# Kernel optimization log

Measured on AMD Instinct MI355X. Metric: run time of the kernel, lower is better.

## Reference

```python
import jax, jax.numpy as jnp
import numpy as np

D = 512  # d_model
B, H, W = 32, 32, 32


def _conv1x1(x, w, b):
    # x: [B,C,H,W], w: [O,C], b: [O] -> [B,O,H,W]
    return jnp.einsum('oc,bchw->bohw', w, x) + b[None, :, None, None]


def setup_inputs() -> dict:
    key = jax.random.key(0)
    ks = jax.random.split(key, 16)
    std = 0.01  # init.normal_(m.weight, 0, 0.01)
    inp = {
        'out0': jax.random.normal(ks[0], (B, D, H, W), jnp.float32),
        'out1': jax.random.normal(ks[1], (B, D, H, W), jnp.float32),
        'out2': jax.random.normal(ks[2], (B, D, H, W), jnp.float32),
        'gamma': jax.random.uniform(ks[3], (1,), jnp.float32),
        'gamma_1': jax.random.uniform(ks[4], (1,), jnp.float32),
        'gamma_2': jax.random.uniform(ks[5], (1,), jnp.float32),
        'W_in1': std * jax.random.normal(ks[6], (D, D), jnp.float32),
        'b_in1': jnp.zeros((D,), jnp.float32),
        'W_in2': std * jax.random.normal(ks[7], (D, D), jnp.float32),
        'b_in2': jnp.zeros((D,), jnp.float32),
        'W_in3': std * jax.random.normal(ks[8], (D, D), jnp.float32),
        'b_in3': jnp.zeros((D,), jnp.float32),
        'W_trans': std * jax.random.normal(ks[9], (3 * D, 3 * D), jnp.float32),
        'b_trans': jnp.zeros((3 * D,), jnp.float32),
        'W_out1': std * jax.random.normal(ks[10], (D, D), jnp.float32),
        'b_out1': jnp.zeros((D,), jnp.float32),
        'W_out2': std * jax.random.normal(ks[11], (D, D), jnp.float32),
        'b_out2': jnp.zeros((D,), jnp.float32),
        'W_out3': std * jax.random.normal(ks[12], (D, D), jnp.float32),
        'b_out3': jnp.zeros((D,), jnp.float32),
    }
    return inp


def reference(out0, out1, out2, gamma, gamma_1, gamma_2,
              W_in1, b_in1, W_in2, b_in2, W_in3, b_in3,
              W_trans, b_trans, W_out1, b_out1, W_out2, b_out2,
              W_out3, b_out3):
    out_sim = gamma[0] * out0
    out_sim_1 = gamma_1[0] * out1
    out_sim_2 = gamma_2[0] * out2
    H_1 = _conv1x1(out_sim, W_in1, b_in1)
    H_2 = _conv1x1(out_sim_1, W_in2, b_in2)
    H_3 = _conv1x1(out_sim_2, W_in3, b_in3)
    H_cat = jnp.concatenate((H_1, H_2, H_3), axis=1)  # [B,3D,H,W]
    H_tra = _conv1x1(H_cat, W_trans, b_trans)
    s0, s1, s2 = H_tra[:, :D], H_tra[:, D:2 * D], H_tra[:, 2 * D:]
    H_4 = jax.nn.sigmoid(_conv1x1(s0, W_out1, b_out1))
    H_5 = jax.nn.sigmoid(_conv1x1(s1, W_out2, b_out2))
    H_6 = jax.nn.sigmoid(_conv1x1(s2, W_out3, b_out3))
    H_st = jnp.stack((H_4, H_5, H_6), axis=0)  # [3,B,D,H,W]
    H_all = jax.nn.softmax(H_st, axis=0)
    fused = H_all[0] * out_sim + H_all[1] * out_sim_1 + H_all[2] * out_sim_2
    return fused
```

## Files before the change

### kernel.cpp

```cpp
#include <hip/hip_runtime.h>
#include <hip/hip_bf16.h>

#define NPIX 32768
#define DCH 512
#define HWSZ 1024
#define WSQ (DCH * DCH)
#define WTR (3 * DCH * 3 * DCH)

typedef __bf16 bf16x8_t __attribute__((ext_vector_type(8)));
typedef float f32x4_t __attribute__((ext_vector_type(4)));
typedef float f32x16_t __attribute__((ext_vector_type(16)));
typedef int i32x4_t __attribute__((ext_vector_type(4)));
typedef int i32x8_t __attribute__((ext_vector_type(8)));
typedef unsigned short u16x8_t __attribute__((ext_vector_type(8)));
typedef unsigned short u16x4_t __attribute__((ext_vector_type(4)));

static __device__ __forceinline__ unsigned short f2bf(float f) {
    return __builtin_bit_cast(unsigned short, __float2bfloat16(f));
}
static __device__ __forceinline__ float bf2f(unsigned short u) {
    unsigned v = (unsigned)u << 16;
    return __builtin_bit_cast(float, v);
}

__global__ __launch_bounds__(256)
void cvt_all(const float* __restrict__ w0, const float* __restrict__ w1,
             const float* __restrict__ w2, const float* __restrict__ w3,
             const float* __restrict__ w4, const float* __restrict__ w5,
             const float* __restrict__ w6, __hip_bfloat16* __restrict__ d,
             const float* __restrict__ b0, const float* __restrict__ b1,
             const float* __restrict__ b2, const float* __restrict__ b3,
             const float* __restrict__ b4, const float* __restrict__ b5,
             float* __restrict__ biasd)
{
    if (blockIdx.x == gridDim.x - 1) {
        for (int idx = threadIdx.x; idx < 3072; idx += 256) {
            const int r = idx >> 9, off = idx & 511;
            const float* s = (r == 0) ? b0 : (r == 1) ? b1 : (r == 2) ? b2
                           : (r == 3) ? b3 : (r == 4) ? b4 : b5;
            biasd[idx] = s[off];
        }
        return;
    }
    const int i = (blockIdx.x * 256 + threadIdx.x) * 4;
    if (i < 3 * WSQ) {
        int r = i >> 18;
        const float* src = (r == 0) ? w0 : ((r == 1) ? w1 : w2);
        int off = i - r * WSQ;
        float4 f = *(const float4*)(src + off);
        u16x4_t v;
        v[0] = f2bf(f.x); v[1] = f2bf(f.y); v[2] = f2bf(f.z); v[3] = f2bf(f.w);
        *(u16x4_t*)((unsigned short*)d + i) = v;
    } else if (i < 3 * WSQ + WTR) {
        int off = i - 3 * WSQ;
        float4 f = *(const float4*)(w3 + off);
        int dw = __builtin_amdgcn_cvt_pk_fp8_f32(f.x, f.y, 0, false);
        dw     = __builtin_amdgcn_cvt_pk_fp8_f32(f.z, f.w, dw, true);
        unsigned char* d8 = (unsigned char*)(d + 3 * WSQ);
        *(int*)(d8 + off) = dw;
    } else {
        int j = i - 3 * WSQ - WTR;
        int r = j >> 18;
        const float* src = (r == 0) ? w4 : ((r == 1) ? w5 : w6);
        int off = j - r * WSQ;
        float4 f = *(const float4*)(src + off);
        u16x4_t v;
        v[0] = f2bf(f.x); v[1] = f2bf(f.y); v[2] = f2bf(f.z); v[3] = f2bf(f.w);
        *(u16x4_t*)((unsigned short*)d + i) = v;
    }
}

__global__ __launch_bounds__(256)
void stage_transpose(const float* __restrict__ x0, const float* __restrict__ x1,
                     const float* __restrict__ x2,
                     const float* __restrict__ gp0, const float* __restrict__ gp1,
                     const float* __restrict__ gp2,
                     __hip_bfloat16* __restrict__ XbT)
{
    __shared__ float tile[64][65];
    const int hw0 = blockIdx.x * 64;
    const int c0  = blockIdx.y * 64;
    const int bz  = blockIdx.z;
    const int br  = bz >> 5;
    const int b   = bz & 31;
    const float* x = (br == 0) ? x0 : ((br == 1) ? x1 : x2);
    const float g  = ((br == 0) ? gp0 : ((br == 1) ? gp1 : gp2))[0];
    const int t = threadIdx.x;

    const int hwi = t & 63;
    const int cb  = t >> 6;
    const float* src = x + (size_t)b * (DCH * HWSZ) + (size_t)c0 * HWSZ + hw0;
#pragma unroll
    for (int i = 0; i < 16; ++i) {
        const int ci = cb + i * 4;
        tile[ci][hwi] = g * src[(size_t)ci * HWSZ + hwi];
    }
    __syncthreads();

    const int hwr = t >> 2;
    const int cch = (t & 3) * 16;
    __hip_bfloat16* dst = XbT + (size_t)((size_t)br * NPIX + b * HWSZ + hw0 + hwr) * DCH + c0 + cch;
    u16x8_t v0, v1;
#pragma unroll
    for (int e = 0; e < 8; ++e) v0[e] = f2bf(tile[cch + e][hwr]);
#pragma unroll
    for (int e = 0; e < 8; ++e) v1[e] = f2bf(tile[cch + 8 + e][hwr]);
    *(u16x8_t*)dst = v0;
    *((u16x8_t*)dst + 1) = v1;
}

__global__ __launch_bounds__(512, 2)
void gemm256(const __hip_bfloat16* __restrict__ A, int lda,
             const __hip_bfloat16* __restrict__ B, int ldb,
             const float* __restrict__ bias,
             __hip_bfloat16* __restrict__ C, int ldc, int coff0,
             int K, int NO, int TPB, int brA, int brB, int bstride,
             int cstride, int trans_out, int cmode)
{
    __shared__ __align__(16) unsigned char smem[131072];
    const int tid  = threadIdx.x;
    const int lane = tid & 63;
    const int wave = tid >> 6;
    const int wm   = wave >> 2;
    const int wn   = wave & 3;
    const int l16  = lane & 15;
    const int l4   = lane >> 4;

    const int per  = gridDim.x >> 3;
    const int flat = (blockIdx.x & 7) * per + (blockIdx.x >> 3);
    const int br   = flat / TPB;
    const int rem  = flat - br * TPB;
    const int nt   = rem / NO;
    const int ot   = rem - nt * NO;
    const int n0 = nt * 256;
    const int o0 = ot * 256;
    const int NT = K >> 6;

    A    += (size_t)br * (size_t)brA;
    B    += (size_t)br * (size_t)brB;
    bias += br * bstride;
    const int coff = coff0 + br * cstride;

    const unsigned xorv = (unsigned)((l16 & 7) << 4);
    unsigned baseA[2], baseB[2];
#pragma unroll
    for (int kk = 0; kk < 2; ++kk) {
        const unsigned ko = ((unsigned)(kk * 64 + l4 * 16)) ^ xorv;
        baseA[kk] = (unsigned)((wm * 128 + l16) * 128) + ko;
        baseB[kk] = 32768u + (unsigned)((wn * 64 + l16) * 128) + ko;
    }

    const int rr  = lane >> 3;
    const int kel = 8 * ((lane & 7) ^ rr);

    auto stageA = [&](int t, int half) {
        const unsigned dst = (unsigned)((t & 1) * 65536 + half * 16384 + wave * 2048);
        const __hip_bfloat16* g = A + (size_t)(n0 + half * 128 + wave * 16 + rr) * lda + t * 64 + kel;
#pragma unroll
        for (int s = 0; s < 2; ++s) {
            __builtin_amdgcn_global_load_lds(
                (const __attribute__((address_space(1))) unsigned int*)(g + (size_t)s * 8 * lda),
                (__attribute__((address_space(3))) unsigned int*)(smem + dst + s * 1024),
                16, 0, 0);
        }
    };
    auto stageB = [&](int t, int half) {
        const unsigned dst = (unsigned)((t & 1) * 65536 + 32768 + half * 16384 + wave * 2048);
        const __hip_bfloat16* g = B + (size_t)(o0 + half * 128 + wave * 16 + rr) * ldb + t * 64 + kel;
#pragma unroll
        for (int s = 0; s < 2; ++s) {
            __builtin_amdgcn_global_load_lds(
                (const __attribute__((address_space(1))) unsigned int*)(g + (size_t)s * 8 * ldb),
                (__attribute__((address_space(3))) unsigned int*)(smem + dst + s * 1024),
                16, 0, 0);
        }
    };

#define DSRO(dst, addr, OFF) \
    asm volatile("ds_read_b128 %0, %1 offset:" #OFF : "=v"(dst) : "v"(addr))
#define BC(x) __builtin_bit_cast(bf16x8_t, x)

    stageA(0, 0); stageA(0, 1); stageB(0, 0); stageB(0, 1);
    stageA(1, 0); stageA(1, 1); stageB(1, 0); stageB(1, 1);
    asm volatile("s_waitcnt vmcnt(8)");
    __builtin_amdgcn_s_barrier();

    f32x4_t aR[4][2], a2[4][2], bA[2][2], bB[2][2];
    f32x4_t acc[8][4];
#pragma unroll
    for (int m = 0; m < 8; ++m)
#pragma unroll
        for (int n = 0; n < 4; ++n) acc[m][n] = (f32x4_t){0.f, 0.f, 0.f, 0.f};

    {
        unsigned a0 = baseA[0], a1 = baseA[1], b0 = baseB[0], b1 = baseB[1];
        DSRO(aR[0][0], a0, 0);    DSRO(aR[1][0], a0, 2048);
        DSRO(aR[2][0], a0, 4096); DSRO(aR[3][0], a0, 6144);
        DSRO(aR[0][1], a1, 0);    DSRO(aR[1][1], a1, 2048);
        DSRO(aR[2][1], a1, 4096); DSRO(aR[3][1], a1, 6144);
        DSRO(bA[0][0], b0, 0);    DSRO(bA[1][0], b0, 2048);
        DSRO(bA[0][1], b1, 0);    DSRO(bA[1][1], b1, 2048);
    }

    unsigned cb = 0;
    for (int t = 0; t < NT; ++t) {
        const unsigned cbn = cb ^ 65536u;
        const unsigned a0 = cb + baseA[0], a1 = cb + baseA[1];
        const unsigned b0 = cb + baseB[0], b1 = cb + baseB[1];

        asm volatile("s_waitcnt lgkmcnt(0)");
        __builtin_amdgcn_sched_barrier(0);
        DSRO(bB[0][0], b0, 4096); DSRO(bB[1][0], b0, 6144);
        DSRO(bB[0][1], b1, 4096); DSRO(bB[1][1], b1, 6144);
        __builtin_amdgcn_sched_barrier(0);
        __builtin_amdgcn_s_setprio(1);
#pragma unroll
        for (int m = 0; m < 4; ++m)
#pragma unroll
            for (int n = 0; n < 2; ++n)
#pragma unroll
                for (int kk = 0; kk < 2; ++kk)
                    acc[m][n] = __builtin_amdgcn_mfma_f32_16x16x32_bf16(BC(aR[m][kk]), BC(bA[n][kk]), acc[m][n], 0, 0, 0);
        __builtin_amdgcn_s_setprio(0);
        __builtin_amdgcn_s_barrier();

        asm volatile("s_waitcnt lgkmcnt(0)");
        __builtin_amdgcn_sched_barrier(0);
        DSRO(a2[0][0], a0, 8192);  DSRO(a2[1][0], a0, 10240);
        DSRO(a2[2][0], a0, 12288); DSRO(a2[3][0], a0, 14336);
        DSRO(a2[0][1], a1, 8192);  DSRO(a2[1][1], a1, 10240);
        DSRO(a2[2][1], a1, 12288); DSRO(a2[3][1], a1, 14336);
        __builtin_amdgcn_sched_barrier(0);
        __builtin_amdgcn_s_setprio(1);
#pragma unroll
        for (int m = 0; m < 4; ++m)
#pragma unroll
            for (int n = 0; n < 2; ++n)
#pragma unroll
                for (int kk = 0; kk < 2; ++kk)
                    acc[m][n + 2] = __builtin_amdgcn_mfma_f32_16x16x32_bf16(BC(aR[m][kk]), BC(bB[n][kk]), acc[m][n + 2], 0, 0, 0);
        __builtin_amdgcn_s_setprio(0);
        __builtin_amdgcn_s_barrier();

        asm volatile("s_waitcnt lgkmcnt(0)");
        __builtin_amdgcn_sched_barrier(0);
        if (t + 2 < NT) { stageB(t + 2, 0); stageB(t + 2, 1); }
        __builtin_amdgcn_sched_barrier(0);
        __builtin_amdgcn_s_setprio(1);
#pragma unroll
        for (int m = 0; m < 4; ++m)
#pragma unroll
            for (int n = 0; n < 2; ++n)
#pragma unroll
                for (int kk = 0; kk < 2; ++kk)
                    acc[m + 4][n] = __builtin_amdgcn_mfma_f32_16x16x32_bf16(BC(a2[m][kk]), BC(bA[n][kk]), acc[m + 4][n], 0, 0, 0);
        __builtin_amdgcn_s_setprio(0);
        if (t + 2 < NT)        { asm volatile("s_waitcnt vmcnt(4)"); }
        else if (t + 2 == NT)  { asm volatile("s_waitcnt vmcnt(0)"); }
        __builtin_amdgcn_s_barrier();

        if (t + 1 < NT) {
            const unsigned na0 = cbn + baseA[0], na1 = cbn + baseA[1];
            const unsigned nb0 = cbn + baseB[0], nb1 = cbn + baseB[1];
            DSRO(aR[0][0], na0, 0);    DSRO(aR[1][0], na0, 2048);
            DSRO(aR[2][0], na0, 4096); DSRO(aR[3][0], na0, 6144);
            DSRO(aR[0][1], na1, 0);    DSRO(aR[1][1], na1, 2048);
            DSRO(aR[2][1], na1, 4096); DSRO(aR[3][1], na1, 6144);
            DSRO(bA[0][0], nb0, 0);    DSRO(bA[1][0], nb0, 2048);
            DSRO(bA[0][1], nb1, 0);    DSRO(bA[1][1], nb1, 2048);
        }
        if (t + 2 < NT) { stageA(t + 2, 0); stageA(t + 2, 1); }
        __builtin_amdgcn_sched_barrier(0);
        __builtin_amdgcn_s_setprio(1);
#pragma unroll
        for (int m = 0; m < 4; ++m)
#pragma unroll
            for (int n = 0; n < 2; ++n)
#pragma unroll
                for (int kk = 0; kk < 2; ++kk)
                    acc[m + 4][n + 2] = __builtin_amdgcn_mfma_f32_16x16x32_bf16(BC(a2[m][kk]), BC(bB[n][kk]), acc[m + 4][n + 2], 0, 0, 0);
        __builtin_amdgcn_s_setprio(0);
        cb = cbn;
    }

    if (!trans_out) {
        if (cmode == 1) {
            unsigned char* C8 = (unsigned char*)C;
#pragma unroll
            for (int n = 0; n < 4; ++n) {
                const int oc = o0 + wn * 64 + n * 16 + l16;
                const float bv = bias[oc];
#pragma unroll
                for (int m = 0; m < 8; ++m) {
                    int dw = __builtin_amdgcn_cvt_pk_fp8_f32(acc[m][n][0] + bv, acc[m][n][1] + bv, 0, false);
                    dw     = __builtin_amdgcn_cvt_pk_fp8_f32(acc[m][n][2] + bv, acc[m][n][3] + bv, dw, true);
                    const int nr = n0 + wm * 128 + m * 16 + l4 * 4;
                    const size_t base = (size_t)nr * ldc + coff + oc;
                    const unsigned u = (unsigned)dw;
                    C8[base]           = (unsigned char)u;
                    C8[base + ldc]     = (unsigned char)(u >> 8);
                    C8[base + 2 * ldc] = (unsigned char)(u >> 16);
                    C8[base + 3 * ldc] = (unsigned char)(u >> 24);
                }
            }
        } else {
#pragma unroll
            for (int n = 0; n < 4; ++n) {
                const int oc = o0 + wn * 64 + n * 16 + l16;
                const float bv = bias[oc];
#pragma unroll
                for (int m = 0; m < 8; ++m)
#pragma unroll
                    for (int r = 0; r < 4; ++r) {
                        const int nr = n0 + wm * 128 + m * 16 + l4 * 4 + r;
                        C[(size_t)nr * ldc + coff + oc] = __float2bfloat16(acc[m][n][r] + bv);
                    }
            }
        }
    } else {
        __syncthreads();
#pragma unroll
        for (int n = 0; n < 4; ++n) {
            const int ocl = wn * 64 + n * 16 + l16;
            const float bv = bias[o0 + ocl];
#pragma unroll
            for (int m = 0; m < 8; ++m)
#pragma unroll
                for (int r = 0; r < 4; ++r) {
                    const int nrow = wm * 128 + m * 16 + l4 * 4 + r;
                    const unsigned phys = (unsigned)nrow * 512u
                        + (((unsigned)ocl * 2u) ^ (((unsigned)(nrow & 7)) << 4));
                    *(unsigned short*)(smem + phys) = f2bf(acc[m][n][r] + bv);
                }
        }
        __syncthreads();
        const int ol = tid >> 1;
        const int nh = (tid & 1) * 128;
        __hip_bfloat16* dst = C + (size_t)(coff + o0 + ol) * ldc + n0 + nh;
#pragma unroll
        for (int j8 = 0; j8 < 16; ++j8) {
            u16x8_t v;
#pragma unroll
            for (int e = 0; e < 8; ++e) {
                const int n2 = nh + j8 * 8 + e;
                v[e] = *(const unsigned short*)(smem + (unsigned)n2 * 512u
                        + ((((unsigned)ol * 2u) ^ ((unsigned)e << 4))));
            }
            *(u16x8_t*)((unsigned short*)dst + j8 * 8) = v;
        }
    }
#undef DSRO
#undef BC
}

__global__ __launch_bounds__(256, 3)
void gemm_f8(const unsigned char* __restrict__ A, int lda,
             const unsigned char* __restrict__ B, int ldb,
             const float* __restrict__ bias,
             __hip_bfloat16* __restrict__ C, int ldc,
             int K, int NO)
{
    __shared__ __align__(16) unsigned char smem[32768];
    const int tid  = threadIdx.x;
    const int lane = tid & 63;
    const int wave = tid >> 6;
    const int wm = wave >> 1, wn = wave & 1;
    const int l31 = lane & 31;
    const int h   = lane >> 5;

    const int per  = gridDim.x >> 3;
    const int flat = (blockIdx.x & 7) * per + (blockIdx.x >> 3);
    const int nt = flat / NO, ot = flat % NO;
    const int n0 = nt * 128, o0 = ot * 128;
    const int NT = K >> 6;

    auto stage = [&](int t, unsigned bufb) {
#pragma unroll
        for (int p = 0; p < 2; ++p) {
            const int f   = tid + p * 256;
            const int row = f >> 2, cidx = f & 3;
            const int gch = ((cidx ^ (row & 3) ^ ((row >> 2) & 3)) << 4);
            const unsigned char* ga = A + (size_t)(n0 + row) * lda + t * 64 + gch;
            __builtin_amdgcn_global_load_lds(
                (const __attribute__((address_space(1))) unsigned int*)ga,
                (__attribute__((address_space(3))) unsigned int*)(smem + bufb + f * 16),
                16, 0, 0);
            const unsigned char* gb = B + (size_t)(o0 + row) * ldb + t * 64 + gch;
            __builtin_amdgcn_global_load_lds(
                (const __attribute__((address_space(1))) unsigned int*)gb,
                (__attribute__((address_space(3))) unsigned int*)(smem + bufb + 8192u + f * 16),
                16, 0, 0);
        }
    };

    f32x16_t acc[2][2];
#pragma unroll
    for (int mf = 0; mf < 2; ++mf)
#pragma unroll
        for (int nf = 0; nf < 2; ++nf)
#pragma unroll
            for (int e = 0; e < 16; ++e) acc[mf][nf][e] = 0.f;

    stage(0, 0);
    __syncthreads();

    for (int t = 0; t < NT; ++t) {
        const unsigned bb = (unsigned)((t & 1) << 14);
        if (t + 1 < NT) stage(t + 1, bb ^ 16384u);

        i32x8_t af[2], bf[2];
#pragma unroll
        for (int mf = 0; mf < 2; ++mf) {
            const int r = wm * 64 + mf * 32 + l31;
            const int s = (r & 3) ^ ((r >> 2) & 3);
            const unsigned base = bb + (unsigned)(r << 6);
            i32x4_t lo = *(const i32x4_t*)(smem + base + ((((h << 1) | 0) ^ s) << 4));
            i32x4_t hi = *(const i32x4_t*)(smem + base + ((((h << 1) | 1) ^ s) << 4));
            af[mf][0] = lo[0]; af[mf][1] = lo[1]; af[mf][2] = lo[2]; af[mf][3] = lo[3];
            af[mf][4] = hi[0]; af[mf][5] = hi[1]; af[mf][6] = hi[2]; af[mf][7] = hi[3];
        }
#pragma unroll
        for (int nf = 0; nf < 2; ++nf) {
            const int r = wn * 64 + nf * 32 + l31;
            const int s = (r & 3) ^ ((r >> 2) & 3);
            const unsigned base = bb + 8192u + (unsigned)(r << 6);
            i32x4_t lo = *(const i32x4_t*)(smem + base + ((((h << 1) | 0) ^ s) << 4));
            i32x4_t hi = *(const i32x4_t*)(smem + base + ((((h << 1) | 1) ^ s) << 4));
            bf[nf][0] = lo[0]; bf[nf][1] = lo[1]; bf[nf][2] = lo[2]; bf[nf][3] = lo[3];
            bf[nf][4] = hi[0]; bf[nf][5] = hi[1]; bf[nf][6] = hi[2]; bf[nf][7] = hi[3];
        }
#pragma unroll
        for (int mf = 0; mf < 2; ++mf)
#pragma unroll
            for (int nf = 0; nf < 2; ++nf)
                acc[mf][nf] = __builtin_amdgcn_mfma_scale_f32_32x32x64_f8f6f4(
                    af[mf], bf[nf], acc[mf][nf],
                    0, 0,
                    0, 0x7F7F7F7F,
                    0, 0x7F7F7F7F);
        __syncthreads();
    }

#pragma unroll
    for (int nf = 0; nf < 2; ++nf) {
        const int col = o0 + wn * 64 + nf * 32 + l31;
        const float bv = bias[col];
#pragma unroll
        for (int mf = 0; mf < 2; ++mf)
#pragma unroll
            for (int rg = 0; rg < 16; ++rg) {
                const int row = n0 + wm * 64 + mf * 32 + (rg & 3) + ((rg >> 2) << 3) + (h << 2);
                C[(size_t)row * ldc + col] = __float2bfloat16(acc[mf][nf][rg] + bv);
            }
    }
}

__global__ __launch_bounds__(256)
void final_v2(const __hip_bfloat16* __restrict__ G,
              const __hip_bfloat16* __restrict__ Xb,
              float* __restrict__ out)
{
    __shared__ float tile[64][68];
    const int n0  = blockIdx.x * 64;
    const int b   = n0 >> 10;
    const int hw0 = n0 & (HWSZ - 1);
    const int t   = threadIdx.x;
    const int nl  = t >> 2;
    const int cg  = (t & 3) * 16;
    const int n   = n0 + nl;
    const unsigned short* gr = (const unsigned short*)G + (size_t)n * 1536;
    const unsigned short* xr = (const unsigned short*)Xb + (size_t)n * 512;
    const int seg = t & 3;
    float* outb = out + (size_t)b * (DCH * HWSZ) + hw0;

    for (int c0 = 0; c0 < DCH; c0 += 64) {
        u16x8_t gl[3][2], xl[3][2];
#pragma unroll
        for (int i = 0; i < 3; ++i) {
            gl[i][0] = *(const u16x8_t*)(gr + i * 512 + c0 + cg);
            gl[i][1] = *(const u16x8_t*)(gr + i * 512 + c0 + cg + 8);
            xl[i][0] = *(const u16x8_t*)(xr + (size_t)i * NPIX * 512 + c0 + cg);
            xl[i][1] = *(const u16x8_t*)(xr + (size_t)i * NPIX * 512 + c0 + cg + 8);
        }
#pragma unroll
        for (int e = 0; e < 16; ++e) {
            const int hh = e >> 3, w = e & 7;
            const float s0 = bf2f(gl[0][hh][w]);
            const float s1 = bf2f(gl[1][hh][w]);
            const float s2 = bf2f(gl[2][hh][w]);
            const float g0 = 1.0f / (1.0f + __expf(-s0));
            const float g1 = 1.0f / (1.0f + __expf(-s1));
            const float g2 = 1.0f / (1.0f + __expf(-s2));
            const float e0 = __expf(g0), e1 = __expf(g1), e2 = __expf(g2);
            const float inv = 1.0f / (e0 + e1 + e2);
            tile[cg + e][nl] = inv * (e0 * bf2f(xl[0][hh][w])
                                    + e1 * bf2f(xl[1][hh][w])
                                    + e2 * bf2f(xl[2][hh][w]));
        }
        __syncthreads();
#pragma unroll
        for (int j4 = 0; j4 < 4; ++j4) {
            float4 v = *(const float4*)&tile[nl][seg * 16 + j4 * 4];
            *(float4*)(outb + (size_t)(c0 + nl) * HWSZ + seg * 16 + j4 * 4) = v;
        }
        __syncthreads();
    }
}

__global__ __launch_bounds__(256)
void final_fuse(const __hip_bfloat16* __restrict__ G,
                const float* __restrict__ x0, const float* __restrict__ x1,
                const float* __restrict__ x2,
                const float* __restrict__ gp0, const float* __restrict__ gp1,
                const float* __restrict__ gp2,
                float* __restrict__ out)
{
    const int n  = blockIdx.x * 256 + threadIdx.x;
    const int b  = n >> 10;
    const int hw = n & (HWSZ - 1);
    const int c0 = blockIdx.y * 64;
    const float ga0 = gp0[0], ga1 = gp1[0], ga2 = gp2[0];
    for (int cc = 0; cc < 64; ++cc) {
        const int c = c0 + cc;
        const float s0 = __bfloat162float(G[(size_t)c * NPIX + n]);
        const float s1 = __bfloat162float(G[(size_t)(c + DCH) * NPIX + n]);
        const float s2 = __bfloat162float(G[(size_t)(c + 2 * DCH) * NPIX + n]);
        const float g0v = 1.0f / (1.0f + __expf(-s0));
        const float g1v = 1.0f / (1.0f + __expf(-s1));
        const float g2v = 1.0f / (1.0f + __expf(-s2));
        const float e0 = __expf(g0v), e1 = __expf(g1v), e2 = __expf(g2v);
        const float inv = 1.0f / (e0 + e1 + e2);
        const size_t xo = (size_t)b * (DCH * HWSZ) + (size_t)c * HWSZ + hw;
        out[xo] = inv * (e0 * ga0 * x0[xo] + e1 * ga1 * x1[xo] + e2 * ga2 * x2[xo]);
    }
}

extern "C" void kernel_launch(void* const* d_in, const int* in_sizes, int n_in,
                              void* d_out, int out_size, void* d_ws, size_t ws_size,
                              hipStream_t stream)
{
    const float* out0   = (const float*)d_in[0];
    const float* out1   = (const float*)d_in[1];
    const float* out2   = (const float*)d_in[2];
    const float* gamma0 = (const float*)d_in[3];
    const float* gamma1 = (const float*)d_in[4];
    const float* gamma2 = (const float*)d_in[5];
    const float* W_in1  = (const float*)d_in[6];
    const float* W_in2  = (const float*)d_in[8];
    const float* W_in3  = (const float*)d_in[10];
    const float* b_in1  = (const float*)d_in[7];
    const float* b_in2  = (const float*)d_in[9];
    const float* b_in3  = (const float*)d_in[11];
    const float* W_tr   = (const float*)d_in[12];
    const float* b_tr   = (const float*)d_in[13];
    const float* W_o1   = (const float*)d_in[14];
    const float* b_o1   = (const float*)d_in[15];
    const float* W_o2   = (const float*)d_in[16];
    const float* b_o2   = (const float*)d_in[17];
    const float* W_o3   = (const float*)d_in[18];
    const float* b_o3   = (const float*)d_in[19];
    float* outp = (float*)d_out;

    unsigned char* ws = (unsigned char*)d_ws;
    const size_t SZ_ACT   = (size_t)3 * NPIX * DCH * 2;
    const size_t WB_BYTES = (size_t)(6 * WSQ + WTR) * 2;
    const size_t NEED3    = 3 * SZ_ACT + WB_BYTES + 4096 * 4;
    const bool   big      = (ws_size >= NEED3);

    __hip_bfloat16* buf0 = (__hip_bfloat16*)ws;
    __hip_bfloat16* buf1 = (__hip_bfloat16*)(ws + SZ_ACT);
    __hip_bfloat16* buf2 = big ? (__hip_bfloat16*)(ws + 2 * SZ_ACT) : buf0;
    unsigned char*  wtop = ws + (big ? 3 : 2) * SZ_ACT;
    __hip_bfloat16* Wb     = (__hip_bfloat16*)wtop;
    __hip_bfloat16* Wb_tr  = Wb + 3 * WSQ;
    unsigned char*  Wtr8   = (unsigned char*)Wb_tr;
    __hip_bfloat16* Wb_o   = Wb_tr + WTR;
    float*          biasWS = (float*)(wtop + WB_BYTES);

    const int CVT_TOTAL = 6 * WSQ + WTR;
    cvt_all<<<CVT_TOTAL / 1024 + 1, 256, 0, stream>>>(
        W_in1, W_in2, W_in3, W_tr, W_o1, W_o2, W_o3, Wb,
        b_in1, b_in2, b_in3, b_o1, b_o2, b_o3, biasWS);

    stage_transpose<<<dim3(16, 8, 96), 256, 0, stream>>>(out0, out1, out2,
                                                         gamma0, gamma1, gamma2, buf0);

    gemm256<<<dim3(768), 512, 0, stream>>>(
        buf0, DCH, Wb, DCH, biasWS,
        buf1, 3 * DCH, 0, DCH, 2, 256, NPIX * DCH, WSQ, DCH, DCH, 0, 1);

    gemm_f8<<<dim3((NPIX / 128) * 12), 256, 0, stream>>>(
        (const unsigned char*)buf1, 3 * DCH, Wtr8, 3 * DCH, b_tr,
        buf2, 3 * DCH, 3 * DCH, 12);

    if (big) {
        gemm256<<<dim3(768), 512, 0, stream>>>(
            buf2, 3 * DCH, Wb_o, DCH, biasWS + 3 * DCH,
            buf1, 3 * DCH, 0, DCH, 2, 256, DCH, WSQ, DCH, DCH, 0, 0);
        final_v2<<<dim3(NPIX / 64), 256, 0, stream>>>(buf1, buf0, outp);
    } else {
        gemm256<<<dim3(768), 512, 0, stream>>>(
            buf0, 3 * DCH, Wb_o, DCH, biasWS + 3 * DCH,
            buf1, NPIX, 0, DCH, 2, 256, DCH, WSQ, DCH, DCH, 1, 0);
        final_fuse<<<dim3(NPIX / 256, DCH / 64), 256, 0, stream>>>(
            buf1, out0, out1, out2, gamma0, gamma1, gamma2, outp);
    }
}
```

Before: 380.9 us.

## Run all three GEMM stages in FP8 with a triple-buffered fp8 GEMM

After: 325.1 us. -14.6%, faster.

```diff
diff --git a/kernel.cpp b/kernel.cpp
--- a/kernel.cpp
+++ b/kernel.cpp
@@ -27,13 +27,16 @@
 void cvt_all(const float* __restrict__ w0, const float* __restrict__ w1,
              const float* __restrict__ w2, const float* __restrict__ w3,
              const float* __restrict__ w4, const float* __restrict__ w5,
-             const float* __restrict__ w6, __hip_bfloat16* __restrict__ d,
+             const float* __restrict__ w6,
+             __hip_bfloat16* __restrict__ d, unsigned char* __restrict__ d8,
              const float* __restrict__ b0, const float* __restrict__ b1,
              const float* __restrict__ b2, const float* __restrict__ b3,
              const float* __restrict__ b4, const float* __restrict__ b5,
              float* __restrict__ biasd)
 {
-    if (blockIdx.x == gridDim.x - 1) {
+    const int NB = (6 * WSQ + WTR) >> 10;
+    const int bid = blockIdx.x;
+    if (bid == 2 * NB) {
         for (int idx = threadIdx.x; idx < 3072; idx += 256) {
             const int r = idx >> 9, off = idx & 511;
             const float* s = (r == 0) ? b0 : (r == 1) ? b1 : (r == 2) ? b2
@@ -42,28 +45,28 @@
         }
         return;
     }
-    const int i = (blockIdx.x * 256 + threadIdx.x) * 4;
+    const bool do8 = (bid >= NB);
+    const int i = ((do8 ? bid - NB : bid) * 256 + threadIdx.x) * 4;
+    const float* src;
+    int off;
     if (i < 3 * WSQ) {
         int r = i >> 18;
-        const float* src = (r == 0) ? w0 : ((r == 1) ? w1 : w2);
-        int off = i - r * WSQ;
-        float4 f = *(const float4*)(src + off);
-        u16x4_t v;
-        v[0] = f2bf(f.x); v[1] = f2bf(f.y); v[2] = f2bf(f.z); v[3] = f2bf(f.w);
-        *(u16x4_t*)((unsigned short*)d + i) = v;
+        src = (r == 0) ? w0 : ((r == 1) ? w1 : w2);
+        off = i - r * WSQ;
     } else if (i < 3 * WSQ + WTR) {
-        int off = i - 3 * WSQ;
-        float4 f = *(const float4*)(w3 + off);
-        int dw = __builtin_amdgcn_cvt_pk_fp8_f32(f.x, f.y, 0, false);
-        dw     = __builtin_amdgcn_cvt_pk_fp8_f32(f.z, f.w, dw, true);
-        unsigned char* d8 = (unsigned char*)(d + 3 * WSQ);
-        *(int*)(d8 + off) = dw;
+        src = w3; off = i - 3 * WSQ;
     } else {
         int j = i - 3 * WSQ - WTR;
         int r = j >> 18;
-        const float* src = (r == 0) ? w4 : ((r == 1) ? w5 : w6);
-        int off = j - r * WSQ;
-        float4 f = *(const float4*)(src + off);
+        src = (r == 0) ? w4 : ((r == 1) ? w5 : w6);
+        off = j - r * WSQ;
+    }
+    float4 f = *(const float4*)(src + off);
+    if (do8) {
+        int dw = __builtin_amdgcn_cvt_pk_fp8_f32(f.x, f.y, 0, false);
+        dw     = __builtin_amdgcn_cvt_pk_fp8_f32(f.z, f.w, dw, true);
+        *(int*)(d8 + i) = dw;
+    } else {
         u16x4_t v;
         v[0] = f2bf(f.x); v[1] = f2bf(f.y); v[2] = f2bf(f.z); v[3] = f2bf(f.w);
         *(u16x4_t*)((unsigned short*)d + i) = v;
@@ -75,7 +78,8 @@
                      const float* __restrict__ x2,
                      const float* __restrict__ gp0, const float* __restrict__ gp1,
                      const float* __restrict__ gp2,
-                     __hip_bfloat16* __restrict__ XbT)
+                     __hip_bfloat16* __restrict__ XbT,
+                     unsigned char* __restrict__ Xb8, int emit8)
 {
     __shared__ float tile[64][65];
     const int hw0 = blockIdx.x * 64;
@@ -99,7 +103,8 @@
 
     const int hwr = t >> 2;
     const int cch = (t & 3) * 16;
-    __hip_bfloat16* dst = XbT + (size_t)((size_t)br * NPIX + b * HWSZ + hw0 + hwr) * DCH + c0 + cch;
+    const size_t nrow = (size_t)br * NPIX + b * HWSZ + hw0 + hwr;
+    __hip_bfloat16* dst = XbT + nrow * DCH + c0 + cch;
     u16x8_t v0, v1;
 #pragma unroll
     for (int e = 0; e < 8; ++e) v0[e] = f2bf(tile[cch + e][hwr]);
@@ -107,260 +112,30 @@
     for (int e = 0; e < 8; ++e) v1[e] = f2bf(tile[cch + 8 + e][hwr]);
     *(u16x8_t*)dst = v0;
     *((u16x8_t*)dst + 1) = v1;
-}
-
-__global__ __launch_bounds__(512, 2)
-void gemm256(const __hip_bfloat16* __restrict__ A, int lda,
-             const __hip_bfloat16* __restrict__ B, int ldb,
-             const float* __restrict__ bias,
-             __hip_bfloat16* __restrict__ C, int ldc, int coff0,
-             int K, int NO, int TPB, int brA, int brB, int bstride,
-             int cstride, int trans_out, int cmode)
-{
-    __shared__ __align__(16) unsigned char smem[131072];
-    const int tid  = threadIdx.x;
-    const int lane = tid & 63;
-    const int wave = tid >> 6;
-    const int wm   = wave >> 2;
-    const int wn   = wave & 3;
-    const int l16  = lane & 15;
-    const int l4   = lane >> 4;
-
-    const int per  = gridDim.x >> 3;
-    const int flat = (blockIdx.x & 7) * per + (blockIdx.x >> 3);
-    const int br   = flat / TPB;
-    const int rem  = flat - br * TPB;
-    const int nt   = rem / NO;
-    const int ot   = rem - nt * NO;
-    const int n0 = nt * 256;
-    const int o0 = ot * 256;
-    const int NT = K >> 6;
-
-    A    += (size_t)br * (size_t)brA;
-    B    += (size_t)br * (size_t)brB;
-    bias += br * bstride;
-    const int coff = coff0 + br * cstride;
-
-    const unsigned xorv = (unsigned)((l16 & 7) << 4);
-    unsigned baseA[2], baseB[2];
-#pragma unroll
-    for (int kk = 0; kk < 2; ++kk) {
-        const unsigned ko = ((unsigned)(kk * 64 + l4 * 16)) ^ xorv;
-        baseA[kk] = (unsigned)((wm * 128 + l16) * 128) + ko;
-        baseB[kk] = 32768u + (unsigned)((wn * 64 + l16) * 128) + ko;
-    }
-
-    const int rr  = lane >> 3;
-    const int kel = 8 * ((lane & 7) ^ rr);
-
-    auto stageA = [&](int t, int half) {
-        const unsigned dst = (unsigned)((t & 1) * 65536 + half * 16384 + wave * 2048);
-        const __hip_bfloat16* g = A + (size_t)(n0 + half * 128 + wave * 16 + rr) * lda + t * 64 + kel;
-#pragma unroll
-        for (int s = 0; s < 2; ++s) {
-            __builtin_amdgcn_global_load_lds(
-                (const __attribute__((address_space(1))) unsigned int*)(g + (size_t)s * 8 * lda),
-                (__attribute__((address_space(3))) unsigned int*)(smem + dst + s * 1024),
-                16, 0, 0);
-        }
-    };
-    auto stageB = [&](int t, int half) {
-        const unsigned dst = (unsigned)((t & 1) * 65536 + 32768 + half * 16384 + wave * 2048);
-        const __hip_bfloat16* g = B + (size_t)(o0 + half * 128 + wave * 16 + rr) * ldb + t * 64 + kel;
-#pragma unroll
-        for (int s = 0; s < 2; ++s) {
-            __builtin_amdgcn_global_load_lds(
-                (const __attribute__((address_space(1))) unsigned int*)(g + (size_t)s * 8 * ldb),
-                (__attribute__((address_space(3))) unsigned int*)(smem + dst + s * 1024),
-                16, 0, 0);
-        }
-    };
-
-#define DSRO(dst, addr, OFF) \
-    asm volatile("ds_read_b128 %0, %1 offset:" #OFF : "=v"(dst) : "v"(addr))
-#define BC(x) __builtin_bit_cast(bf16x8_t, x)
-
-    stageA(0, 0); stageA(0, 1); stageB(0, 0); stageB(0, 1);
-    stageA(1, 0); stageA(1, 1); stageB(1, 0); stageB(1, 1);
-    asm volatile("s_waitcnt vmcnt(8)");
-    __builtin_amdgcn_s_barrier();
-
-    f32x4_t aR[4][2], a2[4][2], bA[2][2], bB[2][2];
-    f32x4_t acc[8][4];
-#pragma unroll
-    for (int m = 0; m < 8; ++m)
-#pragma unroll
-        for (int n = 0; n < 4; ++n) acc[m][n] = (f32x4_t){0.f, 0.f, 0.f, 0.f};
-
-    {
-        unsigned a0 = baseA[0], a1 = baseA[1], b0 = baseB[0], b1 = baseB[1];
-        DSRO(aR[0][0], a0, 0);    DSRO(aR[1][0], a0, 2048);
-        DSRO(aR[2][0], a0, 4096); DSRO(aR[3][0], a0, 6144);
-        DSRO(aR[0][1], a1, 0);    DSRO(aR[1][1], a1, 2048);
-        DSRO(aR[2][1], a1, 4096); DSRO(aR[3][1], a1, 6144);
-        DSRO(bA[0][0], b0, 0);    DSRO(bA[1][0], b0, 2048);
-        DSRO(bA[0][1], b1, 0);    DSRO(bA[1][1], b1, 2048);
-    }
-
-    unsigned cb = 0;
-    for (int t = 0; t < NT; ++t) {
-        const unsigned cbn = cb ^ 65536u;
-        const unsigned a0 = cb + baseA[0], a1 = cb + baseA[1];
-        const unsigned b0 = cb + baseB[0], b1 = cb + baseB[1];
-
-        asm volatile("s_waitcnt lgkmcnt(0)");
-        __builtin_amdgcn_sched_barrier(0);
-        DSRO(bB[0][0], b0, 4096); DSRO(bB[1][0], b0, 6144);
-        DSRO(bB[0][1], b1, 4096); DSRO(bB[1][1], b1, 6144);
-        __builtin_amdgcn_sched_barrier(0);
-        __builtin_amdgcn_s_setprio(1);
-#pragma unroll
-        for (int m = 0; m < 4; ++m)
-#pragma unroll
-            for (int n = 0; n < 2; ++n)
-#pragma unroll
-                for (int kk = 0; kk < 2; ++kk)
-                    acc[m][n] = __builtin_amdgcn_mfma_f32_16x16x32_bf16(BC(aR[m][kk]), BC(bA[n][kk]), acc[m][n], 0, 0, 0);
-        __builtin_amdgcn_s_setprio(0);
-        __builtin_amdgcn_s_barrier();
-
-        asm volatile("s_waitcnt lgkmcnt(0)");
-        __builtin_amdgcn_sched_barrier(0);
-        DSRO(a2[0][0], a0, 8192);  DSRO(a2[1][0], a0, 10240);
-        DSRO(a2[2][0], a0, 12288); DSRO(a2[3][0], a0, 14336);
-        DSRO(a2[0][1], a1, 8192);  DSRO(a2[1][1], a1, 10240);
-        DSRO(a2[2][1], a1, 12288); DSRO(a2[3][1], a1, 14336);
-        __builtin_amdgcn_sched_barrier(0);
-        __builtin_amdgcn_s_setprio(1);
-#pragma unroll
-        for (int m = 0; m < 4; ++m)
-#pragma unroll
-            for (int n = 0; n < 2; ++n)
-#pragma unroll
-                for (int kk = 0; kk < 2; ++kk)
-                    acc[m][n + 2] = __builtin_amdgcn_mfma_f32_16x16x32_bf16(BC(aR[m][kk]), BC(bB[n][kk]), acc[m][n + 2], 0, 0, 0);
-        __builtin_amdgcn_s_setprio(0);
-        __builtin_amdgcn_s_barrier();
-
-        asm volatile("s_waitcnt lgkmcnt(0)");
-        __builtin_amdgcn_sched_barrier(0);
-        if (t + 2 < NT) { stageB(t + 2, 0); stageB(t + 2, 1); }
-        __builtin_amdgcn_sched_barrier(0);
-        __builtin_amdgcn_s_setprio(1);
-#pragma unroll
-        for (int m = 0; m < 4; ++m)
-#pragma unroll
-            for (int n = 0; n < 2; ++n)
-#pragma unroll
-                for (int kk = 0; kk < 2; ++kk)
-                    acc[m + 4][n] = __builtin_amdgcn_mfma_f32_16x16x32_bf16(BC(a2[m][kk]), BC(bA[n][kk]), acc[m + 4][n], 0, 0, 0);
-        __builtin_amdgcn_s_setprio(0);
-        if (t + 2 < NT)        { asm volatile("s_waitcnt vmcnt(4)"); }
-        else if (t + 2 == NT)  { asm volatile("s_waitcnt vmcnt(0)"); }
-        __builtin_amdgcn_s_barrier();
-
-        if (t + 1 < NT) {
-            const unsigned na0 = cbn + baseA[0], na1 = cbn + baseA[1];
-            const unsigned nb0 = cbn + baseB[0], nb1 = cbn + baseB[1];
-            DSRO(aR[0][0], na0, 0);    DSRO(aR[1][0], na0, 2048);
-            DSRO(aR[2][0], na0, 4096); DSRO(aR[3][0], na0, 6144);
-            DSRO(aR[0][1], na1, 0);    DSRO(aR[1][1], na1, 2048);
-            DSRO(aR[2][1], na1, 4096); DSRO(aR[3][1], na1, 6144);
-            DSRO(bA[0][0], nb0, 0);    DSRO(bA[1][0], nb0, 2048);
-            DSRO(bA[0][1], nb1, 0);    DSRO(bA[1][1], nb1, 2048);
-        }
-        if (t + 2 < NT) { stageA(t + 2, 0); stageA(t + 2, 1); }
-        __builtin_amdgcn_sched_barrier(0);
-        __builtin_amdgcn_s_setprio(1);
-#pragma unroll
-        for (int m = 0; m < 4; ++m)
-#pragma unroll
-            for (int n = 0; n < 2; ++n)
-#pragma unroll
-                for (int kk = 0; kk < 2; ++kk)
-                    acc[m + 4][n + 2] = __builtin_amdgcn_mfma_f32_16x16x32_bf16(BC(a2[m][kk]), BC(bB[n][kk]), acc[m + 4][n + 2], 0, 0, 0);
-        __builtin_amdgcn_s_setprio(0);
-        cb = cbn;
-    }
-
-    if (!trans_out) {
-        if (cmode == 1) {
-            unsigned char* C8 = (unsigned char*)C;
-#pragma unroll
-            for (int n = 0; n < 4; ++n) {
-                const int oc = o0 + wn * 64 + n * 16 + l16;
-                const float bv = bias[oc];
-#pragma unroll
-                for (int m = 0; m < 8; ++m) {
-                    int dw = __builtin_amdgcn_cvt_pk_fp8_f32(acc[m][n][0] + bv, acc[m][n][1] + bv, 0, false);
-                    dw     = __builtin_amdgcn_cvt_pk_fp8_f32(acc[m][n][2] + bv, acc[m][n][3] + bv, dw, true);
-                    const int nr = n0 + wm * 128 + m * 16 + l4 * 4;
-                    const size_t base = (size_t)nr * ldc + coff + oc;
-                    const unsigned u = (unsigned)dw;
-                    C8[base]           = (unsigned char)u;
-                    C8[base + ldc]     = (unsigned char)(u >> 8);
-                    C8[base + 2 * ldc] = (unsigned char)(u >> 16);
-                    C8[base + 3 * ldc] = (unsigned char)(u >> 24);
-                }
-            }
-        } else {
-#pragma unroll
-            for (int n = 0; n < 4; ++n) {
-                const int oc = o0 + wn * 64 + n * 16 + l16;
-                const float bv = bias[oc];
-#pragma unroll
-                for (int m = 0; m < 8; ++m)
-#pragma unroll
-                    for (int r = 0; r < 4; ++r) {
-                        const int nr = n0 + wm * 128 + m * 16 + l4 * 4 + r;
-                        C[(size_t)nr * ldc + coff + oc] = __float2bfloat16(acc[m][n][r] + bv);
-                    }
-            }
-        }
-    } else {
-        __syncthreads();
-#pragma unroll
-        for (int n = 0; n < 4; ++n) {
-            const int ocl = wn * 64 + n * 16 + l16;
-            const float bv = bias[o0 + ocl];
-#pragma unroll
-            for (int m = 0; m < 8; ++m)
-#pragma unroll
-                for (int r = 0; r < 4; ++r) {
-                    const int nrow = wm * 128 + m * 16 + l4 * 4 + r;
-                    const unsigned phys = (unsigned)nrow * 512u
-                        + (((unsigned)ocl * 2u) ^ (((unsigned)(nrow & 7)) << 4));
-                    *(unsigned short*)(smem + phys) = f2bf(acc[m][n][r] + bv);
-                }
-        }
-        __syncthreads();
-        const int ol = tid >> 1;
-        const int nh = (tid & 1) * 128;
-        __hip_bfloat16* dst = C + (size_t)(coff + o0 + ol) * ldc + n0 + nh;
-#pragma unroll
-        for (int j8 = 0; j8 < 16; ++j8) {
-            u16x8_t v;
-#pragma unroll
-            for (int e = 0; e < 8; ++e) {
-                const int n2 = nh + j8 * 8 + e;
-                v[e] = *(const unsigned short*)(smem + (unsigned)n2 * 512u
-                        + ((((unsigned)ol * 2u) ^ ((unsigned)e << 4))));
-            }
-            *(u16x8_t*)((unsigned short*)dst + j8 * 8) = v;
-        }
-    }
-#undef DSRO
-#undef BC
+
+    if (emit8) {
+        i32x4_t w;
+#pragma unroll
+        for (int q = 0; q < 4; ++q) {
+            int dw = __builtin_amdgcn_cvt_pk_fp8_f32(tile[cch + 4 * q][hwr],
+                                                     tile[cch + 4 * q + 1][hwr], 0, false);
+            dw     = __builtin_amdgcn_cvt_pk_fp8_f32(tile[cch + 4 * q + 2][hwr],
+                                                     tile[cch + 4 * q + 3][hwr], dw, true);
+            w[q] = dw;
+        }
+        *(i32x4_t*)(Xb8 + nrow * DCH + c0 + cch) = w;
+    }
 }
 
 __global__ __launch_bounds__(256, 3)
 void gemm_f8(const unsigned char* __restrict__ A, int lda,
              const unsigned char* __restrict__ B, int ldb,
              const float* __restrict__ bias,
-             __hip_bfloat16* __restrict__ C, int ldc,
-             int K, int NO)
+             void* __restrict__ Cv, int ldc, int coff0,
+             int K, int NO, int TPB, int brA, int brB,
+             int bstride, int cstride, int cmode)
 {
-    __shared__ __align__(16) unsigned char smem[32768];
+    __shared__ __align__(16) unsigned char smem[49152];
     const int tid  = threadIdx.x;
     const int lane = tid & 63;
     const int wave = tid >> 6;
@@ -370,9 +145,16 @@
 
     const int per  = gridDim.x >> 3;
     const int flat = (blockIdx.x & 7) * per + (blockIdx.x >> 3);
-    const int nt = flat / NO, ot = flat % NO;
+    const int br   = flat / TPB;
+    const int rem  = flat - br * TPB;
+    const int nt = rem / NO, ot = rem % NO;
     const int n0 = nt * 128, o0 = ot * 128;
     const int NT = K >> 6;
+
+    A    += (size_t)br * (size_t)brA;
+    B    += (size_t)br * (size_t)brB;
+    bias += br * bstride;
+    const int coff = coff0 + br * cstride;
 
     auto stage = [&](int t, unsigned bufb) {
 #pragma unroll
@@ -393,6 +175,8 @@
         }
     };
 
+#define DSR(dst, a) asm volatile("ds_read_b128 %0, %1" : "=v"(dst) : "v"(a))
+
     f32x16_t acc[2][2];
 #pragma unroll
     for (int mf = 0; mf < 2; ++mf)
@@ -401,58 +185,324 @@
 #pragma unroll
             for (int e = 0; e < 16; ++e) acc[mf][nf][e] = 0.f;
 
-    stage(0, 0);
-    __syncthreads();
+    stage(0, 0u); stage(1, 16384u);
+    asm volatile("s_waitcnt vmcnt(4)");
+    __builtin_amdgcn_s_barrier();
+
+    unsigned cur = 0u, nxt = 16384u, thr = 32768u;
+    int sA[2], sB[2];
+    unsigned baseA[2], baseB[2];
+#pragma unroll
+    for (int mf = 0; mf < 2; ++mf) {
+        const int r = wm * 64 + mf * 32 + l31;
+        sA[mf] = (r & 3) ^ ((r >> 2) & 3);
+        baseA[mf] = (unsigned)(r << 6);
+        const int rb = wn * 64 + mf * 32 + l31;
+        sB[mf] = (rb & 3) ^ ((rb >> 2) & 3);
+        baseB[mf] = 8192u + (unsigned)(rb << 6);
+    }
 
     for (int t = 0; t < NT; ++t) {
-        const unsigned bb = (unsigned)((t & 1) << 14);
-        if (t + 1 < NT) stage(t + 1, bb ^ 16384u);
+        if (t + 2 < NT) stage(t + 2, thr);
+
+        i32x4_t alo[2], ahi[2], blo[2], bhi[2];
+#pragma unroll
+        for (int mf = 0; mf < 2; ++mf) {
+            DSR(alo[mf], cur + baseA[mf] + ((((h << 1) | 0) ^ sA[mf]) << 4));
+            DSR(ahi[mf], cur + baseA[mf] + ((((h << 1) | 1) ^ sA[mf]) << 4));
+            DSR(blo[mf], cur + baseB[mf] + ((((h << 1) | 0) ^ sB[mf]) << 4));
+            DSR(bhi[mf], cur + baseB[mf] + ((((h << 1) | 1) ^ sB[mf]) << 4));
+        }
+        asm volatile("s_waitcnt lgkmcnt(0)");
+        __builtin_amdgcn_sched_barrier(0);
 
         i32x8_t af[2], bf[2];
 #pragma unroll
         for (int mf = 0; mf < 2; ++mf) {
-            const int r = wm * 64 + mf * 32 + l31;
-            const int s = (r & 3) ^ ((r >> 2) & 3);
-            const unsigned base = bb + (unsigned)(r << 6);
-            i32x4_t lo = *(const i32x4_t*)(smem + base + ((((h << 1) | 0) ^ s) << 4));
-            i32x4_t hi = *(const i32x4_t*)(smem + base + ((((h << 1) | 1) ^ s) << 4));
-            af[mf][0] = lo[0]; af[mf][1] = lo[1]; af[mf][2] = lo[2]; af[mf][3] = lo[3];
-            af[mf][4] = hi[0]; af[mf][5] = hi[1]; af[mf][6] = hi[2]; af[mf][7] = hi[3];
-        }
-#pragma unroll
-        for (int nf = 0; nf < 2; ++nf) {
-            const int r = wn * 64 + nf * 32 + l31;
-            const int s = (r & 3) ^ ((r >> 2) & 3);
-            const unsigned base = bb + 8192u + (unsigned)(r << 6);
-            i32x4_t lo = *(const i32x4_t*)(smem + base + ((((h << 1) | 0) ^ s) << 4));
-            i32x4_t hi = *(const i32x4_t*)(smem + base + ((((h << 1) | 1) ^ s) << 4));
-            bf[nf][0] = lo[0]; bf[nf][1] = lo[1]; bf[nf][2] = lo[2]; bf[nf][3] = lo[3];
-            bf[nf][4] = hi[0]; bf[nf][5] = hi[1]; bf[nf][6] = hi[2]; bf[nf][7] = hi[3];
-        }
+#pragma unroll
+            for (int e = 0; e < 4; ++e) {
+                af[mf][e] = alo[mf][e]; af[mf][e + 4] = ahi[mf][e];
+                bf[mf][e] = blo[mf][e]; bf[mf][e + 4] = bhi[mf][e];
+            }
+        }
+        __builtin_amdgcn_s_setprio(1);
 #pragma unroll
         for (int mf = 0; mf < 2; ++mf)
 #pragma unroll
             for (int nf = 0; nf < 2; ++nf)
                 acc[mf][nf] = __builtin_amdgcn_mfma_scale_f32_32x32x64_f8f6f4(
                     af[mf], bf[nf], acc[mf][nf],
-                    0, 0,
-                    0, 0x7F7F7F7F,
-                    0, 0x7F7F7F7F);
+                    0, 0, 0, 0x7F7F7F7F, 0, 0x7F7F7F7F);
+        __builtin_amdgcn_s_setprio(0);
+
+        if (t + 2 < NT)      { asm volatile("s_waitcnt vmcnt(4)"); }
+        else if (t + 1 < NT) { asm volatile("s_waitcnt vmcnt(0)"); }
+        __builtin_amdgcn_s_barrier();
+        const unsigned tmp = cur; cur = nxt; nxt = thr; thr = tmp;
+    }
+#undef DSR
+
+    if (cmode == 0) {
+        __hip_bfloat16* C = (__hip_bfloat16*)Cv;
+#pragma unroll
+        for (int nf = 0; nf < 2; ++nf) {
+            const int col = o0 + wn * 64 + nf * 32 + l31;
+            const float bv = bias[col];
+#pragma unroll
+            for (int mf = 0; mf < 2; ++mf)
+#pragma unroll
+                for (int rg = 0; rg < 16; ++rg) {
+                    const int row = n0 + wm * 64 + mf * 32 + (rg & 3) + ((rg >> 2) << 3) + (h << 2);
+                    C[(size_t)row * ldc + coff + col] = __float2bfloat16(acc[mf][nf][rg] + bv);
+                }
+        }
+    } else {
+        unsigned char* C8 = (unsigned char*)Cv;
+#pragma unroll
+        for (int nf = 0; nf < 2; ++nf) {
+            const int col = o0 + wn * 64 + nf * 32 + l31;
+            const float bv = bias[col];
+#pragma unroll
+            for (int mf = 0; mf < 2; ++mf)
+#pragma unroll
+                for (int q = 0; q < 4; ++q) {
+                    int dw = __builtin_amdgcn_cvt_pk_fp8_f32(acc[mf][nf][4 * q] + bv,
+                                                             acc[mf][nf][4 * q + 1] + bv, 0, false);
+                    dw     = __builtin_amdgcn_cvt_pk_fp8_f32(acc[mf][nf][4 * q + 2] + bv,
+                                                             acc[mf][nf][4 * q + 3] + bv, dw, true);
+                    const int row = n0 + wm * 64 + mf * 32 + 8 * q + (h << 2);
+                    const size_t base = (size_t)row * ldc + coff + col;
+                    const unsigned u = (unsigned)dw;
+                    C8[base]           = (unsigned char)u;
+                    C8[base + ldc]     = (unsigned char)(u >> 8);
+                    C8[base + 2 * ldc] = (unsigned char)(u >> 16);
+                    C8[base + 3 * ldc] = (unsigned char)(u >> 24);
+                }
+        }
+    }
+}
+
+__global__ __launch_bounds__(512, 2)
+void gemm256(const __hip_bfloat16* __restrict__ A, int lda,
+             const __hip_bfloat16* __restrict__ B, int ldb,
+             const float* __restrict__ bias,
+             __hip_bfloat16* __restrict__ C, int ldc, int coff0,
+             int K, int NO, int TPB, int brA, int brB, int bstride,
+             int cstride, int trans_out)
+{
+    __shared__ __align__(16) unsigned char smem[131072];
+    const int tid  = threadIdx.x;
+    const int lane = tid & 63;
+    const int wave = tid >> 6;
+    const int wm   = wave >> 2;
+    const int wn   = wave & 3;
+    const int l16  = lane & 15;
+    const int l4   = lane >> 4;
+
+    const int per  = gridDim.x >> 3;
+    const int flat = (blockIdx.x & 7) * per + (blockIdx.x >> 3);
+    const int br   = flat / TPB;
+    const int rem  = flat - br * TPB;
+    const int nt   = rem / NO;
+    const int ot   = rem - nt * NO;
+    const int n0 = nt * 256;
+    const int o0 = ot * 256;
+    const int NT = K >> 6;
+
+    A    += (size_t)br * (size_t)brA;
+    B    += (size_t)br * (size_t)brB;
+    bias += br * bstride;
+    const int coff = coff0 + br * cstride;
+
+    const unsigned xorv = (unsigned)((l16 & 7) << 4);
+    unsigned baseA[2], baseB[2];
+#pragma unroll
+    for (int kk = 0; kk < 2; ++kk) {
+        const unsigned ko = ((unsigned)(kk * 64 + l4 * 16)) ^ xorv;
+        baseA[kk] = (unsigned)((wm * 128 + l16) * 128) + ko;
+        baseB[kk] = 32768u + (unsigned)((wn * 64 + l16) * 128) + ko;
+    }
+
+    const int rr  = lane >> 3;
+    const int kel = 8 * ((lane & 7) ^ rr);
+
+    auto stageA = [&](int t, int half) {
+        const unsigned dst = (unsigned)((t & 1) * 65536 + half * 16384 + wave * 2048);
+        const __hip_bfloat16* g = A + (size_t)(n0 + half * 128 + wave * 16 + rr) * lda + t * 64 + kel;
+#pragma unroll
+        for (int s = 0; s < 2; ++s) {
+            __builtin_amdgcn_global_load_lds(
+                (const __attribute__((address_space(1))) unsigned int*)(g + (size_t)s * 8 * lda),
+                (__attribute__((address_space(3))) unsigned int*)(smem + dst + s * 1024),
+                16, 0, 0);
+        }
+    };
+    auto stageB = [&](int t, int half) {
+        const unsigned dst = (unsigned)((t & 1) * 65536 + 32768 + half * 16384 + wave * 2048);
+        const __hip_bfloat16* g = B + (size_t)(o0 + half * 128 + wave * 16 + rr) * ldb + t * 64 + kel;
+#pragma unroll
+        for (int s = 0; s < 2; ++s) {
+            __builtin_amdgcn_global_load_lds(
+                (const __attribute__((address_space(1))) unsigned int*)(g + (size_t)s * 8 * ldb),
+                (__attribute__((address_space(3))) unsigned int*)(smem + dst + s * 1024),
+                16, 0, 0);
+        }
+    };
+
+#define DSRO(dst, addr, OFF) \
+    asm volatile("ds_read_b128 %0, %1 offset:" #OFF : "=v"(dst) : "v"(addr))
+#define BC(x) __builtin_bit_cast(bf16x8_t, x)
+
+    stageA(0, 0); stageA(0, 1); stageB(0, 0); stageB(0, 1);
+    stageA(1, 0); stageA(1, 1); stageB(1, 0); stageB(1, 1);
+    asm volatile("s_waitcnt vmcnt(8)");
+    __builtin_amdgcn_s_barrier();
+
+    f32x4_t aR[4][2], a2[4][2], bA[2][2], bB[2][2];
+    f32x4_t acc[8][4];
+#pragma unroll
+    for (int m = 0; m < 8; ++m)
+#pragma unroll
+        for (int n = 0; n < 4; ++n) acc[m][n] = (f32x4_t){0.f, 0.f, 0.f, 0.f};
+
+    {
+        unsigned a0 = baseA[0], a1 = baseA[1], b0 = baseB[0], b1 = baseB[1];
+        DSRO(aR[0][0], a0, 0);    DSRO(aR[1][0], a0, 2048);
+        DSRO(aR[2][0], a0, 4096); DSRO(aR[3][0], a0, 6144);
+        DSRO(aR[0][1], a1, 0);    DSRO(aR[1][1], a1, 2048);
+        DSRO(aR[2][1], a1, 4096); DSRO(aR[3][1], a1, 6144);
+        DSRO(bA[0][0], b0, 0);    DSRO(bA[1][0], b0, 2048);
+        DSRO(bA[0][1], b1, 0);    DSRO(bA[1][1], b1, 2048);
+    }
+
+    unsigned cb = 0;
+    for (int t = 0; t < NT; ++t) {
+        const unsigned cbn = cb ^ 65536u;
+        const unsigned a0 = cb + baseA[0], a1 = cb + baseA[1];
+        const unsigned b0 = cb + baseB[0], b1 = cb + baseB[1];
+
+        asm volatile("s_waitcnt lgkmcnt(0)");
+        __builtin_amdgcn_sched_barrier(0);
+        DSRO(bB[0][0], b0, 4096); DSRO(bB[1][0], b0, 6144);
+        DSRO(bB[0][1], b1, 4096); DSRO(bB[1][1], b1, 6144);
+        __builtin_amdgcn_sched_barrier(0);
+        __builtin_amdgcn_s_setprio(1);
+#pragma unroll
+        for (int m = 0; m < 4; ++m)
+#pragma unroll
+            for (int n = 0; n < 2; ++n)
+#pragma unroll
+                for (int kk = 0; kk < 2; ++kk)
+                    acc[m][n] = __builtin_amdgcn_mfma_f32_16x16x32_bf16(BC(aR[m][kk]), BC(bA[n][kk]), acc[m][n], 0, 0, 0);
+        __builtin_amdgcn_s_setprio(0);
+        __builtin_amdgcn_s_barrier();
+
+        asm volatile("s_waitcnt lgkmcnt(0)");
+        __builtin_amdgcn_sched_barrier(0);
+        DSRO(a2[0][0], a0, 8192);  DSRO(a2[1][0], a0, 10240);
+        DSRO(a2[2][0], a0, 12288); DSRO(a2[3][0], a0, 14336);
+        DSRO(a2[0][1], a1, 8192);  DSRO(a2[1][1], a1, 10240);
+        DSRO(a2[2][1], a1, 12288); DSRO(a2[3][1], a1, 14336);
+        __builtin_amdgcn_sched_barrier(0);
+        __builtin_amdgcn_s_setprio(1);
+#pragma unroll
+        for (int m = 0; m < 4; ++m)
+#pragma unroll
+            for (int n = 0; n < 2; ++n)
+#pragma unroll
+                for (int kk = 0; kk < 2; ++kk)
+                    acc[m][n + 2] = __builtin_amdgcn_mfma_f32_16x16x32_bf16(BC(aR[m][kk]), BC(bB[n][kk]), acc[m][n + 2], 0, 0, 0);
+        __builtin_amdgcn_s_setprio(0);
+        __builtin_amdgcn_s_barrier();
+
+        asm volatile("s_waitcnt lgkmcnt(0)");
+        __builtin_amdgcn_sched_barrier(0);
+        if (t + 2 < NT) { stageB(t + 2, 0); stageB(t + 2, 1); }
+        __builtin_amdgcn_sched_barrier(0);
+        __builtin_amdgcn_s_setprio(1);
+#pragma unroll
+        for (int m = 0; m < 4; ++m)
+#pragma unroll
+            for (int n = 0; n < 2; ++n)
+#pragma unroll
+                for (int kk = 0; kk < 2; ++kk)
+                    acc[m + 4][n] = __builtin_amdgcn_mfma_f32_16x16x32_bf16(BC(a2[m][kk]), BC(bA[n][kk]), acc[m + 4][n], 0, 0, 0);
+        __builtin_amdgcn_s_setprio(0);
+        if (t + 2 < NT)        { asm volatile("s_waitcnt vmcnt(4)"); }
+        else if (t + 2 == NT)  { asm volatile("s_waitcnt vmcnt(0)"); }
+        __builtin_amdgcn_s_barrier();
+
+        if (t + 1 < NT) {
+            const unsigned na0 = cbn + baseA[0], na1 = cbn + baseA[1];
+            const unsigned nb0 = cbn + baseB[0], nb1 = cbn + baseB[1];
+            DSRO(aR[0][0], na0, 0);    DSRO(aR[1][0], na0, 2048);
+            DSRO(aR[2][0], na0, 4096); DSRO(aR[3][0], na0, 6144);
+            DSRO(aR[0][1], na1, 0);    DSRO(aR[1][1], na1, 2048);
+            DSRO(aR[2][1], na1, 4096); DSRO(aR[3][1], na1, 6144);
+            DSRO(bA[0][0], nb0, 0);    DSRO(bA[1][0], nb0, 2048);
+            DSRO(bA[0][1], nb1, 0);    DSRO(bA[1][1], nb1, 2048);
+        }
+        if (t + 2 < NT) { stageA(t + 2, 0); stageA(t + 2, 1); }
+        __builtin_amdgcn_sched_barrier(0);
+        __builtin_amdgcn_s_setprio(1);
+#pragma unroll
+        for (int m = 0; m < 4; ++m)
+#pragma unroll
+            for (int n = 0; n < 2; ++n)
+#pragma unroll
+                for (int kk = 0; kk < 2; ++kk)
+                    acc[m + 4][n + 2] = __builtin_amdgcn_mfma_f32_16x16x32_bf16(BC(a2[m][kk]), BC(bB[n][kk]), acc[m + 4][n + 2], 0, 0, 0);
+        __builtin_amdgcn_s_setprio(0);
+        cb = cbn;
+    }
+
+    if (!trans_out) {
+#pragma unroll
+        for (int n = 0; n < 4; ++n) {
+            const int oc = o0 + wn * 64 + n * 16 + l16;
+            const float bv = bias[oc];
+#pragma unroll
+            for (int m = 0; m < 8; ++m)
+#pragma unroll
+                for (int r = 0; r < 4; ++r) {
+                    const int nr = n0 + wm * 128 + m * 16 + l4 * 4 + r;
+                    C[(size_t)nr * ldc + coff + oc] = __float2bfloat16(acc[m][n][r] + bv);
+                }
+        }
+    } else {
         __syncthreads();
-    }
-
-#pragma unroll
-    for (int nf = 0; nf < 2; ++nf) {
-        const int col = o0 + wn * 64 + nf * 32 + l31;
-        const float bv = bias[col];
-#pragma unroll
-        for (int mf = 0; mf < 2; ++mf)
-#pragma unroll
-            for (int rg = 0; rg < 16; ++rg) {
-                const int row = n0 + wm * 64 + mf * 32 + (rg & 3) + ((rg >> 2) << 3) + (h << 2);
-                C[(size_t)row * ldc + col] = __float2bfloat16(acc[mf][nf][rg] + bv);
+#pragma unroll
+        for (int n = 0; n < 4; ++n) {
+            const int ocl = wn * 64 + n * 16 + l16;
+            const float bv = bias[o0 + ocl];
+#pragma unroll
+            for (int m = 0; m < 8; ++m)
+#pragma unroll
+                for (int r = 0; r < 4; ++r) {
+                    const int nrow = wm * 128 + m * 16 + l4 * 4 + r;
+                    const unsigned phys = (unsigned)nrow * 512u
+                        + (((unsigned)ocl * 2u) ^ (((unsigned)(nrow & 7)) << 4));
+                    *(unsigned short*)(smem + phys) = f2bf(acc[m][n][r] + bv);
+                }
+        }
+        __syncthreads();
+        const int ol = tid >> 1;
+        const int nh = (tid & 1) * 128;
+        __hip_bfloat16* dst = C + (size_t)(coff + o0 + ol) * ldc + n0 + nh;
+#pragma unroll
+        for (int j8 = 0; j8 < 16; ++j8) {
+            u16x8_t v;
+#pragma unroll
+            for (int e = 0; e < 8; ++e) {
+                const int n2 = nh + j8 * 8 + e;
+                v[e] = *(const unsigned short*)(smem + (unsigned)n2 * 512u
+                        + ((((unsigned)ol * 2u) ^ ((unsigned)e << 4))));
             }
-    }
+            *(u16x8_t*)((unsigned short*)dst + j8 * 8) = v;
+        }
+    }
+#undef DSRO
+#undef BC
 }
 
 __global__ __launch_bounds__(256)
@@ -562,46 +612,56 @@
     float* outp = (float*)d_out;
 
     unsigned char* ws = (unsigned char*)d_ws;
-    const size_t SZ_ACT   = (size_t)3 * NPIX * DCH * 2;
-    const size_t WB_BYTES = (size_t)(6 * WSQ + WTR) * 2;
-    const size_t NEED3    = 3 * SZ_ACT + WB_BYTES + 4096 * 4;
-    const bool   big      = (ws_size >= NEED3);
+    const size_t SZ_ACT  = (size_t)3 * NPIX * DCH * 2;
+    const size_t SZ_ACT8 = (size_t)3 * NPIX * DCH;
+    const size_t WB_BF16 = (size_t)(6 * WSQ + WTR) * 2;
+    const size_t WB_FP8  = (size_t)(6 * WSQ + WTR);
+    const size_t NEED    = 2 * SZ_ACT + SZ_ACT8 + WB_BF16 + WB_FP8 + 16384;
+    const bool   big     = (ws_size >= NEED);
 
     __hip_bfloat16* buf0 = (__hip_bfloat16*)ws;
-    __hip_bfloat16* buf1 = (__hip_bfloat16*)(ws + SZ_ACT);
-    __hip_bfloat16* buf2 = big ? (__hip_bfloat16*)(ws + 2 * SZ_ACT) : buf0;
-    unsigned char*  wtop = ws + (big ? 3 : 2) * SZ_ACT;
+    unsigned char*  P8   = ws + SZ_ACT;
+    unsigned char*  Q    = ws + SZ_ACT + SZ_ACT8;
+    unsigned char*  wtop = big ? (ws + 2 * SZ_ACT + SZ_ACT8) : (ws + 2 * SZ_ACT);
     __hip_bfloat16* Wb     = (__hip_bfloat16*)wtop;
     __hip_bfloat16* Wb_tr  = Wb + 3 * WSQ;
-    unsigned char*  Wtr8   = (unsigned char*)Wb_tr;
     __hip_bfloat16* Wb_o   = Wb_tr + WTR;
-    float*          biasWS = (float*)(wtop + WB_BYTES);
-
-    const int CVT_TOTAL = 6 * WSQ + WTR;
-    cvt_all<<<CVT_TOTAL / 1024 + 1, 256, 0, stream>>>(
-        W_in1, W_in2, W_in3, W_tr, W_o1, W_o2, W_o3, Wb,
+    unsigned char*  Wf8    = wtop + WB_BF16;
+    unsigned char*  Win8   = Wf8;
+    unsigned char*  Wtr8   = Wf8 + 3 * WSQ;
+    unsigned char*  Wo8    = Wf8 + 3 * WSQ + WTR;
+    float*          biasWS = (float*)(wtop + WB_BF16 + WB_FP8);
+
+    const int NB = (6 * WSQ + WTR) >> 10;
+    cvt_all<<<2 * NB + 1, 256, 0, stream>>>(
+        W_in1, W_in2, W_in3, W_tr, W_o1, W_o2, W_o3, Wb, Wf8,
         b_in1, b_in2, b_in3, b_o1, b_o2, b_o3, biasWS);
 
-    stage_transpose<<<dim3(16, 8, 96), 256, 0, stream>>>(out0, out1, out2,
-                                                         gamma0, gamma1, gamma2, buf0);
-
-    gemm256<<<dim3(768), 512, 0, stream>>>(
-        buf0, DCH, Wb, DCH, biasWS,
-        buf1, 3 * DCH, 0, DCH, 2, 256, NPIX * DCH, WSQ, DCH, DCH, 0, 1);
-
-    gemm_f8<<<dim3((NPIX / 128) * 12), 256, 0, stream>>>(
-        (const unsigned char*)buf1, 3 * DCH, Wtr8, 3 * DCH, b_tr,
-        buf2, 3 * DCH, 3 * DCH, 12);
+    stage_transpose<<<dim3(16, 8, 96), 256, 0, stream>>>(
+        out0, out1, out2, gamma0, gamma1, gamma2, buf0, P8, big ? 1 : 0);
 
     if (big) {
+        gemm_f8<<<dim3(3072), 256, 0, stream>>>(
+            P8, DCH, Win8, DCH, biasWS, Q, 3 * DCH, 0,
+            DCH, 4, 1024, NPIX * DCH, WSQ, DCH, DCH, 1);
+        gemm_f8<<<dim3(3072), 256, 0, stream>>>(
+            Q, 3 * DCH, Wtr8, 3 * DCH, b_tr, P8, 3 * DCH, 0,
+            3 * DCH, 12, 3072, 0, 0, 0, 0, 1);
+        gemm_f8<<<dim3(3072), 256, 0, stream>>>(
+            P8, 3 * DCH, Wo8, DCH, biasWS + 3 * DCH, Q, 3 * DCH, 0,
+            DCH, 4, 1024, DCH, WSQ, DCH, DCH, 0);
+        final_v2<<<dim3(NPIX / 64), 256, 0, stream>>>((const __hip_bfloat16*)Q, buf0, outp);
+    } else {
+        __hip_bfloat16* buf1 = (__hip_bfloat16*)(ws + SZ_ACT);
         gemm256<<<dim3(768), 512, 0, stream>>>(
-            buf2, 3 * DCH, Wb_o, DCH, biasWS + 3 * DCH,
-            buf1, 3 * DCH, 0, DCH, 2, 256, DCH, WSQ, DCH, DCH, 0, 0);
-        final_v2<<<dim3(NPIX / 64), 256, 0, stream>>>(buf1, buf0, outp);
-    } else {
+            buf0, DCH, Wb, DCH, biasWS,
+            buf1, 3 * DCH, 0, DCH, 2, 256, NPIX * DCH, WSQ, DCH, DCH, 0);
+        gemm256<<<dim3(768), 512, 0, stream>>>(
+            buf1, 3 * DCH, Wb_tr, 3 * DCH, b_tr,
+            buf0, 3 * DCH, 0, 3 * DCH, 6, 768, 0, 0, 0, 0, 0);
         gemm256<<<dim3(768), 512, 0, stream>>>(
             buf0, 3 * DCH, Wb_o, DCH, biasWS + 3 * DCH,
-            buf1, NPIX, 0, DCH, 2, 256, DCH, WSQ, DCH, DCH, 1, 0);
+            buf1, NPIX, 0, DCH, 2, 256, DCH, WSQ, DCH, DCH, 1);
         final_fuse<<<dim3(NPIX / 256, DCH / 64), 256, 0, stream>>>(
             buf1, out0, out1, out2, gamma0, gamma1, gamma2, outp);
     }
```
